# Optimization experiments

Measured on AMD Instinct MI355X. Metric: run time of the kernel, lower is better.

Reference implementation:

```python
import jax, jax.numpy as jnp
import numpy as np


def fwht(x):
    """Fast Walsh-Hadamard transform over last axis (power-of-2 length), normalized by 1/sqrt(n).
    Matches matmul_hadU with K=1 (pure Hadamard rotation)."""
    orig_shape = x.shape
    n = orig_shape[-1]
    x = x.reshape(-1, n)
    h = 1
    while h < n:
        x = x.reshape(-1, n // (2 * h), 2, h)
        a = x[:, :, 0, :]
        b = x[:, :, 1, :]
        x = jnp.stack([a + b, a - b], axis=2)
        h *= 2
    x = x.reshape(orig_shape)
    return x * (1.0 / np.sqrt(n)).astype(np.float32)


def setup_inputs() -> dict:
    key = jax.random.key(0)
    k1, k2, k3, k4, k5 = jax.random.split(key, 5)
    B, S, n, m = 2, 2048, 4096, 4096
    CODEBOOK = 65536  # 2^16 E8P codes, each decoding an 8-dim lattice point
    inp = jax.random.normal(k1, (B, S, n), dtype=jnp.float32)
    # SU/SV are random sign-like diagonal rescales in QuIP; use unit-variance floats here
    SU = jax.random.normal(k2, (n,), dtype=jnp.float32)
    SV = jax.random.normal(k3, (m,), dtype=jnp.float32)
    grid = jax.random.normal(k4, (CODEBOOK, 8), dtype=jnp.float32) * 0.1
    Qidxs = jax.random.randint(k5, (m, n // 8), 0, CODEBOOK, dtype=jnp.int32)
    return {"input": inp, "SU": SU, "SV": SV, "grid": grid, "Qidxs": Qidxs}


def reference(input, SU, SV, grid, Qidxs):
    n = SU.shape[0]
    m = SV.shape[0]
    x = input.reshape(-1, n) * SU          # diagonal rescale by SU
    x = fwht(x)                             # left Hadamard rotation
    # Dequantize packed E8P codebook: each 16-bit code -> 8 weights
    W = grid[Qidxs].reshape(m, n)           # [m, n]
    x = x @ W.T                             # dense GEMM against dequantized weight
    x = fwht(x)                             # right Hadamard rotation
    x = x * SV                              # diagonal rescale by SV
    return x.reshape(input.shape[:-1] + (m,))
```

## Files before the change

kernel.cpp:

```cpp
#include <hip/hip_runtime.h>
#include <stdint.h>

typedef __bf16 bf16x8 __attribute__((ext_vector_type(8)));
typedef float f32x4 __attribute__((ext_vector_type(4)));

__device__ __forceinline__ unsigned int f2bf(float f) {
  unsigned int u = __float_as_uint(f);
  return (u + 0x7fffu + ((u >> 16) & 1u)) >> 16;
}
__device__ __forceinline__ unsigned int pack2(float a, float b) {
  return f2bf(a) | (f2bf(b) << 16);
}

__device__ __forceinline__ void fwht16(float v[16]) {
#pragma unroll
  for (int s = 0; s < 4; ++s) {
    const int h = 1 << s;
#pragma unroll
    for (int i = 0; i < 16; ++i) {
      if (!(i & h)) {
        float a = v[i], b = v[i ^ h];
        v[i] = a + b;
        v[i ^ h] = a - b;
      }
    }
  }
}

#define LP(i) ((i) + ((i) >> 5))

__global__ void __launch_bounds__(256) k_fwht_in(const float* __restrict__ X,
                                                 const float* __restrict__ SU,
                                                 unsigned short* __restrict__ Xh) {
  __shared__ float lds[4224];
  const int t = threadIdx.x;
  const size_t row = blockIdx.x;
  const float4* xr = (const float4*)(X + row * 4096);
  const float4* su = (const float4*)SU;
  float v[16];
#pragma unroll
  for (int q = 0; q < 4; ++q) {
    float4 a = xr[4 * t + q], s = su[4 * t + q];
    v[4 * q + 0] = a.x * s.x;
    v[4 * q + 1] = a.y * s.y;
    v[4 * q + 2] = a.z * s.z;
    v[4 * q + 3] = a.w * s.w;
  }
  fwht16(v);
#pragma unroll
  for (int q = 0; q < 4; ++q) {
    int i0 = 16 * t + 4 * q;
    *(float4*)&lds[LP(i0)] = make_float4(v[4 * q], v[4 * q + 1], v[4 * q + 2], v[4 * q + 3]);
  }
  __syncthreads();
  const int b = ((t >> 4) << 8) | (t & 15);
#pragma unroll
  for (int j = 0; j < 16; ++j) { int i = b + 16 * j; v[j] = lds[LP(i)]; }
  fwht16(v);
#pragma unroll
  for (int j = 0; j < 16; ++j) { int i = b + 16 * j; lds[LP(i)] = v[j]; }
  __syncthreads();
#pragma unroll
  for (int j = 0; j < 16; ++j) { int i = t + 256 * j; v[j] = lds[LP(i)]; }
  fwht16(v);
  unsigned short* orow = Xh + row * 4096;
#pragma unroll
  for (int j = 0; j < 16; ++j)
    orow[t + 256 * j] = (unsigned short)f2bf(v[j] * 0.015625f);
}

__global__ void __launch_bounds__(256) k_decompress(const int* __restrict__ Qidxs,
                                                    const float* __restrict__ G,
                                                    unsigned short* __restrict__ Wh) {
  int e = blockIdx.x * 256 + threadIdx.x;
  int idx = Qidxs[e];
  const float4* g = (const float4*)(G + (size_t)idx * 8);
  float4 a = g[0], b = g[1];
  uint4 o;
  o.x = pack2(a.x, a.y);
  o.y = pack2(a.z, a.w);
  o.z = pack2(b.x, b.y);
  o.w = pack2(b.z, b.w);
  ((uint4*)Wh)[e] = o;
}

__device__ __forceinline__ void gl2lds16(const unsigned short* g, unsigned short* l) {
  __builtin_amdgcn_global_load_lds(
      (const __attribute__((address_space(1))) void*)g,
      (__attribute__((address_space(3))) void*)l, 16, 0, 0);
}

#define BARX() __builtin_amdgcn_s_barrier()
#define SCHEDB() __builtin_amdgcn_sched_barrier(0)
#define WAITV4() asm volatile("s_waitcnt vmcnt(4)" ::: "memory")
#define WAITV2() asm volatile("s_waitcnt vmcnt(2)" ::: "memory")

#define RD_A(dst, mm)                                                          \
  _Pragma("unroll") for (int kh = 0; kh < 2; ++kh)                             \
      dst[kh] = *(const bf16x8*)&sAp[(((wr) << 7) + ((mm) << 4) + frow) * 64 + \
                                     ((((kh << 2) + jb) ^ sw) << 3)];
#define RD_B()                                                                 \
  _Pragma("unroll") for (int n = 0; n < 4; ++n)                                \
      _Pragma("unroll") for (int kh = 0; kh < 2; ++kh)                         \
          bq[n][kh] = *(const bf16x8*)&sBp[(((wc) << 6) + (n << 4) + frow) * 64 + \
                                           ((((kh << 2) + jb) ^ sw) << 3)];
#define MF(mm, buf)                                                            \
  _Pragma("unroll") for (int n = 0; n < 4; ++n)                                \
      _Pragma("unroll") for (int kh = 0; kh < 2; ++kh)                         \
          acc[(mm)][n] = __builtin_amdgcn_mfma_f32_16x16x32_bf16(              \
              buf[kh], bq[n][kh], acc[(mm)][n], 0, 0, 0);

__global__ void __launch_bounds__(512, 2)
k_gemm_bt(const unsigned short* __restrict__ A,
          const unsigned short* __restrict__ B,
          float* __restrict__ C) {
  const int K = 4096, N = 4096;
  __shared__ unsigned short sA[2][256 * 64];
  __shared__ unsigned short sB[2][256 * 64];
  const int tid = threadIdx.x;
  const int lane = tid & 63;
  const int wave = tid >> 6;
  const int wr = wave >> 2;
  const int wc = wave & 3;
  const int frow = lane & 15;
  const int jb = lane >> 4;
  const int sw = frow & 7;
  const int bn = blockIdx.x, bm = blockIdx.y;
  const size_t rowA0 = (size_t)bm * 256;
  const size_t rowB0 = (size_t)bn * 256;

  f32x4 acc[8][4] = {};

  auto stage = [&](const unsigned short* __restrict__ G, size_t row0,
                   unsigned short* dst, int h, int ktile) {
    const int kt = (ktile < 64 ? ktile : 0) << 6;
#pragma unroll
    for (int l = 0; l < 2; ++l) {
      const int c = (l << 9) + tid;
      const int r = c >> 3;
      const int jg = (c & 7) ^ (r & 7);
      gl2lds16(G + (row0 + (size_t)((h << 7) + r)) * K + kt + (jg << 3),
               dst + (h << 13) + (c << 3));
    }
  };

  auto group = [&](int p, int gA, int gB) {
    const unsigned short* sAp = sA[p];
    const unsigned short* sBp = sB[p];
    unsigned short* sAn = (unsigned short*)sA[p ^ 1];
    unsigned short* sBn = (unsigned short*)sB[p];
    bf16x8 bq[4][2];
    bf16x8 aX[2], aY[2];
    RD_B();
    RD_A(aX, 0);
    RD_A(aY, 1);
    stage(A, rowA0, sAn, 0, gA);
    BARX(); SCHEDB();
    __builtin_amdgcn_s_setprio(1);
    MF(0, aX);
    RD_A(aX, 2);
    MF(1, aY);
    __builtin_amdgcn_s_setprio(0);
    BARX(); SCHEDB();
    RD_A(aY, 3);
    stage(A, rowA0, sAn, 1, gA);
    BARX(); SCHEDB();
    __builtin_amdgcn_s_setprio(1);
    MF(2, aX);
    RD_A(aX, 4);
    MF(3, aY);
    __builtin_amdgcn_s_setprio(0);
    WAITV4(); SCHEDB();
    BARX(); SCHEDB();
    RD_A(aY, 5);
    stage(B, rowB0, sBn, 0, gB);
    BARX(); SCHEDB();
    __builtin_amdgcn_s_setprio(1);
    MF(4, aX);
    RD_A(aX, 6);
    MF(5, aY);
    __builtin_amdgcn_s_setprio(0);
    WAITV2(); SCHEDB();
    BARX(); SCHEDB();
    RD_A(aY, 7);
    stage(B, rowB0, sBn, 1, gB);
    BARX(); SCHEDB();
    __builtin_amdgcn_s_setprio(1);
    MF(6, aX);
    MF(7, aY);
    __builtin_amdgcn_s_setprio(0);
    BARX(); SCHEDB();
  };

  stage(B, rowB0, sB[0], 0, 0);
  stage(B, rowB0, sB[0], 1, 0);
  stage(A, rowA0, sA[0], 0, 0);
  stage(A, rowA0, sA[0], 1, 0);
  stage(B, rowB0, sB[1], 0, 1);
  stage(B, rowB0, sB[1], 1, 1);
  WAITV4();
  BARX();
  SCHEDB();

#pragma unroll 1
  for (int i = 0; i < 32; ++i) {
    group(0, 2 * i + 1, 2 * i + 2);
    group(1, 2 * i + 2, 2 * i + 3);
  }

  const int rbase = bm * 256 + (wr << 7) + (jb << 2);
  const int cbase = bn * 256 + (wc << 6) + frow;
#pragma unroll
  for (int m = 0; m < 8; ++m)
#pragma unroll
    for (int n = 0; n < 4; ++n) {
      float* cp = C + (size_t)(rbase + (m << 4)) * N + cbase + (n << 4);
#pragma unroll
      for (int r = 0; r < 4; ++r) cp[(size_t)r * N] = acc[m][n][r];
    }
}

__global__ void __launch_bounds__(256) k_fwht_out(float* __restrict__ Y,
                                                  const float* __restrict__ SV) {
  __shared__ float lds[4224];
  const int t = threadIdx.x;
  const size_t row = blockIdx.x;
  float* yrow = Y + row * 4096;
  const float4* yr = (const float4*)yrow;
  float v[16];
#pragma unroll
  for (int q = 0; q < 4; ++q) {
    float4 a = yr[4 * t + q];
    v[4 * q + 0] = a.x;
    v[4 * q + 1] = a.y;
    v[4 * q + 2] = a.z;
    v[4 * q + 3] = a.w;
  }
  fwht16(v);
#pragma unroll
  for (int q = 0; q < 4; ++q) {
    int i0 = 16 * t + 4 * q;
    *(float4*)&lds[LP(i0)] = make_float4(v[4 * q], v[4 * q + 1], v[4 * q + 2], v[4 * q + 3]);
  }
  __syncthreads();
  const int b = ((t >> 4) << 8) | (t & 15);
#pragma unroll
  for (int j = 0; j < 16; ++j) { int i = b + 16 * j; v[j] = lds[LP(i)]; }
  fwht16(v);
#pragma unroll
  for (int j = 0; j < 16; ++j) { int i = b + 16 * j; lds[LP(i)] = v[j]; }
  __syncthreads();
#pragma unroll
  for (int j = 0; j < 16; ++j) { int i = t + 256 * j; v[j] = lds[LP(i)]; }
  fwht16(v);
#pragma unroll
  for (int j = 0; j < 16; ++j) {
    int i = t + 256 * j;
    yrow[i] = v[j] * SV[i] * 0.015625f;
  }
}

extern "C" void kernel_launch(void* const* d_in, const int* in_sizes, int n_in,
                              void* d_out, int out_size, void* d_ws, size_t ws_size,
                              hipStream_t stream) {
  const float* X     = (const float*)d_in[0];
  const float* SU    = (const float*)d_in[1];
  const float* SV    = (const float*)d_in[2];
  const float* G     = (const float*)d_in[3];
  const int*   Qidxs = (const int*)d_in[4];
  float* out = (float*)d_out;

  unsigned short* Xh = (unsigned short*)d_ws;
  unsigned short* Wh = Xh + (size_t)4096 * 4096;

  k_fwht_in<<<4096, 256, 0, stream>>>(X, SU, Xh);
  k_decompress<<<(4096 * 512) / 256, 256, 0, stream>>>(Qidxs, G, Wh);
  k_gemm_bt<<<dim3(16, 16), 512, 0, stream>>>(Xh, Wh, out);
  k_fwht_out<<<4096, 256, 0, stream>>>(out, SV);
}
```

Measured before the change: 272.0 us.

## Merge input FWHT and decompress kernels; triple-buffer A fragments in GEMM

Folds the weight-decompress kernel into the input FWHT kernel as extra blocks, removing one launch and letting the two independent prep phases overlap. In the GEMM inner group, A fragments now rotate through three register buffers instead of two, so LDS reads run further ahead of the MFMAs, and the intermediate vmcnt(2) wait is dropped for a single vmcnt(4) wait at the end. This costs more VGPRs, which may hurt occupancy under the 512x2 launch bounds. Relaxing the wait placement also risks reading B stages before their loads have landed.

```diff
diff --git a/kernel.cpp b/kernel.cpp
--- a/kernel.cpp
+++ b/kernel.cpp
@@ -29,11 +29,27 @@
 
 #define LP(i) ((i) + ((i) >> 5))
 
-__global__ void __launch_bounds__(256) k_fwht_in(const float* __restrict__ X,
-                                                 const float* __restrict__ SU,
-                                                 unsigned short* __restrict__ Xh) {
+__global__ void __launch_bounds__(256) k_prep(const float* __restrict__ X,
+                                              const float* __restrict__ SU,
+                                              unsigned short* __restrict__ Xh,
+                                              const int* __restrict__ Qidxs,
+                                              const float* __restrict__ G,
+                                              unsigned short* __restrict__ Wh) {
   __shared__ float lds[4224];
   const int t = threadIdx.x;
+  if (blockIdx.x >= 4096) {
+    int e = (blockIdx.x - 4096) * 256 + t;
+    int idx = Qidxs[e];
+    const float4* g = (const float4*)(G + (size_t)idx * 8);
+    float4 a = g[0], b = g[1];
+    uint4 o;
+    o.x = pack2(a.x, a.y);
+    o.y = pack2(a.z, a.w);
+    o.z = pack2(b.x, b.y);
+    o.w = pack2(b.z, b.w);
+    ((uint4*)Wh)[e] = o;
+    return;
+  }
   const size_t row = blockIdx.x;
   const float4* xr = (const float4*)(X + row * 4096);
   const float4* su = (const float4*)SU;
@@ -69,21 +85,6 @@
     orow[t + 256 * j] = (unsigned short)f2bf(v[j] * 0.015625f);
 }
 
-__global__ void __launch_bounds__(256) k_decompress(const int* __restrict__ Qidxs,
-                                                    const float* __restrict__ G,
-                                                    unsigned short* __restrict__ Wh) {
-  int e = blockIdx.x * 256 + threadIdx.x;
-  int idx = Qidxs[e];
-  const float4* g = (const float4*)(G + (size_t)idx * 8);
-  float4 a = g[0], b = g[1];
-  uint4 o;
-  o.x = pack2(a.x, a.y);
-  o.y = pack2(a.z, a.w);
-  o.z = pack2(b.x, b.y);
-  o.w = pack2(b.z, b.w);
-  ((uint4*)Wh)[e] = o;
-}
-
 __device__ __forceinline__ void gl2lds16(const unsigned short* g, unsigned short* l) {
   __builtin_amdgcn_global_load_lds(
       (const __attribute__((address_space(1))) void*)g,
@@ -93,7 +94,6 @@
 #define BARX() __builtin_amdgcn_s_barrier()
 #define SCHEDB() __builtin_amdgcn_sched_barrier(0)
 #define WAITV4() asm volatile("s_waitcnt vmcnt(4)" ::: "memory")
-#define WAITV2() asm volatile("s_waitcnt vmcnt(2)" ::: "memory")
 
 #define RD_A(dst, mm)                                                          \
   _Pragma("unroll") for (int kh = 0; kh < 2; ++kh)                             \
@@ -150,45 +150,44 @@
     unsigned short* sAn = (unsigned short*)sA[p ^ 1];
     unsigned short* sBn = (unsigned short*)sB[p];
     bf16x8 bq[4][2];
-    bf16x8 aX[2], aY[2];
+    bf16x8 r0[2], r1[2], r2[2];
+    RD_A(r0, 0);
     RD_B();
-    RD_A(aX, 0);
-    RD_A(aY, 1);
+    RD_A(r1, 1);
+    RD_A(r2, 2);
     stage(A, rowA0, sAn, 0, gA);
     BARX(); SCHEDB();
     __builtin_amdgcn_s_setprio(1);
-    MF(0, aX);
-    RD_A(aX, 2);
-    MF(1, aY);
-    __builtin_amdgcn_s_setprio(0);
-    BARX(); SCHEDB();
-    RD_A(aY, 3);
+    MF(0, r0);
+    RD_A(r0, 3);
+    MF(1, r1);
+    __builtin_amdgcn_s_setprio(0);
+    BARX(); SCHEDB();
+    RD_A(r1, 4);
     stage(A, rowA0, sAn, 1, gA);
     BARX(); SCHEDB();
     __builtin_amdgcn_s_setprio(1);
-    MF(2, aX);
-    RD_A(aX, 4);
-    MF(3, aY);
+    MF(2, r2);
+    RD_A(r2, 5);
+    MF(3, r0);
+    __builtin_amdgcn_s_setprio(0);
+    BARX(); SCHEDB();
+    RD_A(r0, 6);
+    stage(B, rowB0, sBn, 0, gB);
+    BARX(); SCHEDB();
+    __builtin_amdgcn_s_setprio(1);
+    MF(4, r1);
+    RD_A(r1, 7);
+    MF(5, r2);
+    __builtin_amdgcn_s_setprio(0);
+    BARX(); SCHEDB();
+    stage(B, rowB0, sBn, 1, gB);
+    BARX(); SCHEDB();
+    __builtin_amdgcn_s_setprio(1);
+    MF(6, r0);
+    MF(7, r1);
     __builtin_amdgcn_s_setprio(0);
     WAITV4(); SCHEDB();
-    BARX(); SCHEDB();
-    RD_A(aY, 5);
-    stage(B, rowB0, sBn, 0, gB);
-    BARX(); SCHEDB();
-    __builtin_amdgcn_s_setprio(1);
-    MF(4, aX);
-    RD_A(aX, 6);
-    MF(5, aY);
-    __builtin_amdgcn_s_setprio(0);
-    WAITV2(); SCHEDB();
-    BARX(); SCHEDB();
-    RD_A(aY, 7);
-    stage(B, rowB0, sBn, 1, gB);
-    BARX(); SCHEDB();
-    __builtin_amdgcn_s_setprio(1);
-    MF(6, aX);
-    MF(7, aY);
-    __builtin_amdgcn_s_setprio(0);
     BARX(); SCHEDB();
   };
 
@@ -273,8 +272,7 @@
   unsigned short* Xh = (unsigned short*)d_ws;
   unsigned short* Wh = Xh + (size_t)4096 * 4096;
 
-  k_fwht_in<<<4096, 256, 0, stream>>>(X, SU, Xh);
-  k_decompress<<<(4096 * 512) / 256, 256, 0, stream>>>(Qidxs, G, Wh);
+  k_prep<<<4096 + 8192, 256, 0, stream>>>(X, SU, Xh, Qidxs, G, Wh);
   k_gemm_bt<<<dim3(16, 16), 512, 0, stream>>>(Xh, Wh, out);
   k_fwht_out<<<4096, 256, 0, stream>>>(out, SV);
 }
```

Measured after the change: 268.9 us. Within noise of the previous version (-1.1%).
